# Performance work log

Measured on AMD Instinct MI355X. Metric: run time of the kernel, lower is better.

## Reference

```python
import jax, jax.numpy as jnp
import numpy as np

EPS_DISC = 1e-9  # matches mamba_discretization denominator epsilon


def setup_inputs() -> dict:
    key = jax.random.key(0)
    ks = jax.random.split(key, 12)
    L, D, N, W = 2048, 1024, 16, 3
    s = 0.02  # small init scale to keep softplus/exp well-behaved
    u_seq = jax.random.normal(ks[0], (L, D), jnp.float32)
    # A_log = log(-A) with A = randn*0.1 - 1.0  -> log of a value near 1
    A_log = jnp.log(jnp.clip(1.0 - 0.1 * jax.random.normal(ks[1], (N,), jnp.float32), 0.5, 1.5))
    dt_w = jax.random.normal(ks[2], (D, D), jnp.float32) * s
    dt_b = jax.random.normal(ks[3], (D,), jnp.float32) * s
    B_w = jax.random.normal(ks[4], (N, D), jnp.float32) * s
    B_b = jax.random.normal(ks[5], (N,), jnp.float32) * s
    C_w = jax.random.normal(ks[6], (N, D), jnp.float32) * s
    C_b = jax.random.normal(ks[7], (N,), jnp.float32) * s
    D_w = jnp.ones((D,), jnp.float32)
    scale = jnp.ones((), jnp.float32)
    init_w = jax.random.normal(ks[8], (D * N, D * W), jnp.float32) * s
    init_b = jax.random.normal(ks[9], (D * N,), jnp.float32) * s
    return {"u_seq": u_seq, "A_log": A_log, "dt_w": dt_w, "dt_b": dt_b,
            "B_w": B_w, "B_b": B_b, "C_w": C_w, "C_b": C_b,
            "D_w": D_w, "scale": scale, "init_w": init_w, "init_b": init_b}


def reference(u_seq, A_log, dt_w, dt_b, B_w, B_b, C_w, C_b, D_w, scale, init_w, init_b):
    L, D = u_seq.shape
    N = A_log.shape[0]
    init_window = init_w.shape[1] // D
    # Initial state h0 = init_estimator(u[:W].flatten()).view(D, N)
    u_prefix = u_seq[:init_window].reshape(-1)
    h0 = (u_prefix @ init_w.T + init_b).reshape(D, N)
    # Input-dependent SSM parameters (all L timesteps at once)
    dt = jax.nn.softplus(u_seq @ dt_w.T + dt_b)           # [L, D]
    B = u_seq @ B_w.T + B_b                               # [L, N]
    C = u_seq @ C_w.T + C_b                               # [L, N]
    A = -jnp.exp(A_log)                                   # [N]
    dtA = dt[:, :, None] * A                              # [L, D, N]
    dA = jnp.exp(dtA)                                     # [L, D, N]
    dB = jnp.expm1(dtA) / (dtA + EPS_DISC) * B[:, None, :]  # ZOH discretization
    Bu = dB * u_seq[:, :, None]                           # [L, D, N]

    # Sequential selective-scan recurrence: h_t = dA_t * h_{t-1} + Bu_t
    def step(h, inp):
        dA_t, Bu_t = inp
        h = dA_t * h + Bu_t
        return h, h

    _, h_hist = jax.lax.scan(step, h0, (dA, Bu))          # [L, D, N]
    y_raw = jnp.einsum('ln,ldn->ld', C, h_hist) + D_w * u_seq
    return jax.nn.softplus(y_raw) * jnp.maximum(scale, 0.5)
```

## Files before the change

### kernel.cpp

```cpp
#include <hip/hip_runtime.h>
#include <hip/hip_bf16.h>

typedef __attribute__((ext_vector_type(8))) short short8v;
typedef __attribute__((ext_vector_type(4))) float f32x4;

#define L_SEQ 2048
#define D_DIM 1024
#define N_DIM 16
#define T_CHUNK 32
#define NCHUNK (L_SEQ / T_CHUNK)
#define EPS_DISC 1e-9f

__device__ __forceinline__ float softplusf(float x) {
    return (x > 15.f) ? x : __logf(1.f + __expf(x));
}

__device__ __forceinline__ unsigned short f2bf(float f) {
    unsigned int u = __float_as_uint(f);
    u += 0x7FFFu + ((u >> 16) & 1u);
    return (unsigned short)(u >> 16);
}
__device__ __forceinline__ unsigned int pack2(float a, float b) {
    return (unsigned int)f2bf(a) | ((unsigned int)f2bf(b) << 16);
}
__device__ __forceinline__ float dot4(float4 a, float4 b) {
    return a.x * b.x + a.y * b.y + a.z * b.z + a.w * b.w;
}
__device__ __forceinline__ float dot4v(f32x4 a, f32x4 b) {
    return a.x * b.x + a.y * b.y + a.z * b.z + a.w * b.w;
}

__global__ __launch_bounds__(256, 4) void k_params(const float* __restrict__ u,
                                                   const float* __restrict__ dt_w,
                                                   const float* __restrict__ dt_b,
                                                   const float* __restrict__ B_w,
                                                   const float* __restrict__ B_b,
                                                   const float* __restrict__ C_w,
                                                   const float* __restrict__ C_b,
                                                   const float* __restrict__ init_w,
                                                   const float* __restrict__ init_b,
                                                   float* __restrict__ dt,
                                                   float* __restrict__ Bm,
                                                   float* __restrict__ Cm,
                                                   float* __restrict__ h0) {
    __shared__ unsigned int smem[3072];
    const int b = blockIdx.x;
    const int t = threadIdx.x;
    const int r3 = b % 3;

    if (r3 != 2) {
        const int m = 2 * (b / 3) + r3;
        const int wv = t >> 6, lane = t & 63;
        const int r0 = m * 16 + wv * 4;
        const f32x4* u4 = (const f32x4*)u;
        f32x4 uu[12];
#pragma unroll
        for (int i = 0; i < 12; ++i) uu[i] = u4[i * 64 + lane];
        float rs[4];
#pragma unroll
        for (int j = 0; j < 4; ++j) {
            const f32x4* w4 = (const f32x4*)init_w + (size_t)(r0 + j) * 768;
            f32x4 wr[12];
#pragma unroll
            for (int i = 0; i < 12; ++i)
                wr[i] = __builtin_nontemporal_load(&w4[i * 64 + lane]);
            float s0 = 0.f, s1 = 0.f, s2 = 0.f;
#pragma unroll
            for (int i = 0; i < 4; ++i) {
                s0 += dot4v(wr[i], uu[i]);
                s1 += dot4v(wr[i + 4], uu[i + 4]);
                s2 += dot4v(wr[i + 8], uu[i + 8]);
            }
            rs[j] = s0 + s1 + s2;
        }
#pragma unroll
        for (int j = 0; j < 4; ++j)
#pragma unroll
            for (int mm = 32; mm >= 1; mm >>= 1) rs[j] += __shfl_xor(rs[j], mm);
        if (lane == 0) {
#pragma unroll
            for (int j = 0; j < 4; ++j) h0[r0 + j] = rs[j] + init_b[r0 + j];
        }
        return;
    }

    const int s = b / 3;
    if (s < 256) {
        unsigned int* As = smem;
        unsigned int* Bs = smem + 1024;
        const int bm = s & 31;
        const int bn = s >> 5;
        const int lane = t & 63;
        const int wn   = t >> 6;
        const int lrow = lane & 15, lq = lane >> 4;

        const int arow = t >> 2, aq = t & 3;
        const int brow = t >> 1, bhalf = t & 1;

        const float* uptr = u + (bm * 64 + arow) * 1024 + aq * 8;
        const float* wptr = dt_w + (bn * 128 + brow) * 1024 + bhalf * 16;

        f32x4 acc[4][2];
#pragma unroll
        for (int mi = 0; mi < 4; ++mi)
#pragma unroll
            for (int ni = 0; ni < 2; ++ni) acc[mi][ni] = (f32x4){0.f, 0.f, 0.f, 0.f};

        for (int k0 = 0; k0 < 1024; k0 += 32) {
            __syncthreads();
            {
                const float4* p = (const float4*)(uptr + k0);
                float4 a0 = p[0], a1 = p[1];
                uint4 ca = make_uint4(pack2(a0.x, a0.y), pack2(a0.z, a0.w),
                                      pack2(a1.x, a1.y), pack2(a1.z, a1.w));
                const int akb = aq ^ ((arow >> 1) & 3);
                *(uint4*)&As[arow * 16 + akb * 4] = ca;

                const float4* q = (const float4*)(wptr + k0);
                float4 b0 = q[0], b1 = q[1], b2 = q[2], b3 = q[3];
                uint4 d0 = make_uint4(pack2(b0.x, b0.y), pack2(b0.z, b0.w),
                                      pack2(b1.x, b1.y), pack2(b1.z, b1.w));
                uint4 d1 = make_uint4(pack2(b2.x, b2.y), pack2(b2.z, b2.w),
                                      pack2(b3.x, b3.y), pack2(b3.z, b3.w));
                const int bswz = (brow >> 1) & 3;
                const int kb0 = (bhalf * 2) ^ bswz, kb1 = (bhalf * 2 + 1) ^ bswz;
                *(uint4*)&Bs[brow * 16 + kb0 * 4] = d0;
                *(uint4*)&Bs[brow * 16 + kb1 * 4] = d1;
            }
            __syncthreads();
            short8v af[4], bf[2];
#pragma unroll
            for (int mi = 0; mi < 4; ++mi) {
                const int ar = mi * 16 + lrow;
                const int kb = lq ^ ((ar >> 1) & 3);
                af[mi] = *(const short8v*)&As[ar * 16 + kb * 4];
            }
#pragma unroll
            for (int ni = 0; ni < 2; ++ni) {
                const int br = wn * 32 + ni * 16 + lrow;
                const int kb = lq ^ ((br >> 1) & 3);
                bf[ni] = *(const short8v*)&Bs[br * 16 + kb * 4];
            }
#pragma unroll
            for (int mi = 0; mi < 4; ++mi)
#pragma unroll
                for (int ni = 0; ni < 2; ++ni)
                    acc[mi][ni] = __builtin_amdgcn_mfma_f32_16x16x32_bf16(af[mi], bf[ni], acc[mi][ni], 0, 0, 0);
        }

#pragma unroll
        for (int mi = 0; mi < 4; ++mi)
#pragma unroll
            for (int ni = 0; ni < 2; ++ni) {
                const int cg = bn * 128 + wn * 32 + ni * 16 + lrow;
                const float bv = dt_b[cg];
#pragma unroll
                for (int j = 0; j < 4; ++j) {
                    const int rg = bm * 64 + mi * 16 + lq * 4 + j;
                    dt[rg * 1024 + cg] = softplusf(acc[mi][ni][j] + bv);
                }
            }
    } else {
        const int s2 = s - 256;
        const int wv = t >> 6, lane = t & 63;
#pragma unroll
        for (int rep = 0; rep < 2; ++rep) {
            const int l = s2 * 8 + wv * 2 + rep;
            const float4* u4 = (const float4*)(u + l * 1024);
            float4 ur[4];
#pragma unroll
            for (int i = 0; i < 4; ++i) ur[i] = u4[i * 64 + lane];
#pragma unroll 4
            for (int c = 0; c < 32; ++c) {
                const float4* wr = (const float4*)((c < 16) ? (B_w + c * 1024)
                                                            : (C_w + (c - 16) * 1024));
                float sv = 0.f;
#pragma unroll
                for (int i = 0; i < 4; ++i) sv += dot4(ur[i], wr[i * 64 + lane]);
#pragma unroll
                for (int off = 32; off > 0; off >>= 1) sv += __shfl_down(sv, off);
                if (lane == 0) {
                    if (c < 16) Bm[l * 16 + c] = sv + B_b[c];
                    else        Cm[l * 16 + (c - 16)] = sv + C_b[c - 16];
                }
            }
        }
    }
}

__global__ __launch_bounds__(256) void k_p1(const float* __restrict__ dt,
                                            const float* __restrict__ Bm,
                                            const float* __restrict__ u,
                                            const float* __restrict__ A_log,
                                            float* __restrict__ ap,
                                            float* __restrict__ hl) {
    const int t    = threadIdx.x;
    const int c    = blockIdx.x >> 3;
    const int dblk = blockIdx.x & 7;
    const int dd   = t >> 1;
    const int nh   = t & 1;
    const int d    = dblk * 128 + dd;
    float An[8];
#pragma unroll
    for (int n = 0; n < 8; ++n) An[n] = -__expf(A_log[nh * 8 + n]);
    float h[8], p[8];
#pragma unroll
    for (int n = 0; n < 8; ++n) { h[n] = 0.f; p[n] = 1.f; }

    const int l0 = c * T_CHUNK;
    for (int i = 0; i < T_CHUNK; ++i) {
        const int l = l0 + i;
        const float dtld = dt[l * D_DIM + d];
        const float uld  = u[l * D_DIM + d];
        const float4 b0 = *(const float4*)&Bm[l * 16 + nh * 8];
        const float4 b1 = *(const float4*)&Bm[l * 16 + nh * 8 + 4];
        auto body = [&](int n, float bn) {
            const float x = dtld * An[n];
            const float e = __expf(x);
            const float coef = (e - 1.f) * __builtin_amdgcn_rcpf(x + EPS_DISC);
            const float bu = coef * bn * uld;
            p[n] *= e;
            h[n] = fmaf(e, h[n], bu);
        };
        body(0, b0.x); body(1, b0.y); body(2, b0.z); body(3, b0.w);
        body(4, b1.x); body(5, b1.y); body(6, b1.z); body(7, b1.w);
    }
    const int base = c * (D_DIM * N_DIM) + d * 16 + nh * 8;
    *(float4*)&ap[base + 0] = make_float4(p[0], p[1], p[2], p[3]);
    *(float4*)&ap[base + 4] = make_float4(p[4], p[5], p[6], p[7]);
    *(float4*)&hl[base + 0] = make_float4(h[0], h[1], h[2], h[3]);
    *(float4*)&hl[base + 4] = make_float4(h[4], h[5], h[6], h[7]);
}

__global__ __launch_bounds__(64) void k_p2(const float* __restrict__ h0,
                                           float* __restrict__ ap,
                                           const float* __restrict__ hl) {
    const int ch = blockIdx.x * 64 + threadIdx.x;
    float h = h0[ch];
#pragma unroll 8
    for (int c = 0; c < NCHUNK; ++c) {
        const int idx = c * (D_DIM * N_DIM) + ch;
        const float a = ap[idx];
        const float b = hl[idx];
        ap[idx] = h;
        h = fmaf(a, h, b);
    }
}

__global__ __launch_bounds__(256) void k_p3(const float* __restrict__ dt,
                                            const float* __restrict__ Bm,
                                            const float* __restrict__ Cm,
                                            const float* __restrict__ u,
                                            const float* __restrict__ A_log,
                                            const float* __restrict__ hstart,
                                            const float* __restrict__ D_w,
                                            const float* __restrict__ scale,
                                            float* __restrict__ out) {
    const int t    = threadIdx.x;
    const int c    = blockIdx.x >> 3;
    const int dblk = blockIdx.x & 7;
    const int dd   = t >> 1;
    const int nh   = t & 1;
    const int d    = dblk * 128 + dd;
    float An[8];
#pragma unroll
    for (int n = 0; n < 8; ++n) An[n] = -__expf(A_log[nh * 8 + n]);
    float h[8];
    const int base = c * (D_DIM * N_DIM) + d * 16 + nh * 8;
    {
        float4 h0v = *(const float4*)&hstart[base + 0];
        float4 h1v = *(const float4*)&hstart[base + 4];
        h[0] = h0v.x; h[1] = h0v.y; h[2] = h0v.z; h[3] = h0v.w;
        h[4] = h1v.x; h[5] = h1v.y; h[6] = h1v.z; h[7] = h1v.w;
    }
    const float scl = fmaxf(scale[0], 0.5f);
    const float dw = D_w[d];
    const int l0 = c * T_CHUNK;
    for (int i = 0; i < T_CHUNK; ++i) {
        const int l = l0 + i;
        const float dtld = dt[l * D_DIM + d];
        const float uld  = u[l * D_DIM + d];
        const float4 b0 = *(const float4*)&Bm[l * 16 + nh * 8];
        const float4 b1 = *(const float4*)&Bm[l * 16 + nh * 8 + 4];
        const float4 c0 = *(const float4*)&Cm[l * 16 + nh * 8];
        const float4 c1 = *(const float4*)&Cm[l * 16 + nh * 8 + 4];
        float y = 0.f;
        auto body = [&](int n, float bn, float cn) {
            const float x = dtld * An[n];
            const float e = __expf(x);
            const float coef = (e - 1.f) * __builtin_amdgcn_rcpf(x + EPS_DISC);
            const float bu = coef * bn * uld;
            h[n] = fmaf(e, h[n], bu);
            y = fmaf(cn, h[n], y);
        };
        body(0, b0.x, c0.x); body(1, b0.y, c0.y); body(2, b0.z, c0.z); body(3, b0.w, c0.w);
        body(4, b1.x, c1.x); body(5, b1.y, c1.y); body(6, b1.z, c1.z); body(7, b1.w, c1.w);
        y += __shfl_xor(y, 1);
        if (nh == 0) {
            const float yv = fmaf(dw, uld, y);
            out[l * D_DIM + d] = softplusf(yv) * scl;
        }
    }
}

extern "C" void kernel_launch(void* const* d_in, const int* in_sizes, int n_in,
                              void* d_out, int out_size, void* d_ws, size_t ws_size,
                              hipStream_t stream) {
    const float* u      = (const float*)d_in[0];
    const float* A_log  = (const float*)d_in[1];
    const float* dt_w   = (const float*)d_in[2];
    const float* dt_b   = (const float*)d_in[3];
    const float* B_w    = (const float*)d_in[4];
    const float* B_b    = (const float*)d_in[5];
    const float* C_w    = (const float*)d_in[6];
    const float* C_b    = (const float*)d_in[7];
    const float* D_w    = (const float*)d_in[8];
    const float* scale  = (const float*)d_in[9];
    const float* init_w = (const float*)d_in[10];
    const float* init_b = (const float*)d_in[11];
    float* out = (float*)d_out;

    float* ws = (float*)d_ws;
    float* dt = ws;
    float* Bm = dt + 2097152;
    float* Cm = Bm + 32768;
    float* h0 = Cm + 32768;
    float* ap = h0 + 16384;
    float* hl = ap + 1048576;

    hipLaunchKernelGGL(k_params, dim3(1536), dim3(256), 0, stream,
                       u, dt_w, dt_b, B_w, B_b, C_w, C_b, init_w, init_b,
                       dt, Bm, Cm, h0);
    hipLaunchKernelGGL(k_p1, dim3(512), dim3(256), 0, stream, dt, Bm, u, A_log, ap, hl);
    hipLaunchKernelGGL(k_p2, dim3(256), dim3(64), 0, stream, h0, ap, hl);
    hipLaunchKernelGGL(k_p3, dim3(512), dim3(256), 0, stream, dt, Bm, Cm, u, A_log, ap, D_w, scale, out);
}
```

Baseline: 119.2 us.

## Stream init_w through LDS with async double-buffered global_load_lds for h0 GEMV

Replaces the interleaved block mapping (two init-GEMV blocks per dt-GEMM block) with contiguous block ranges, and rewrites the h0 GEMV so each block handles a 16-row slab. Weight rows are copied into a double-buffered LDS staging area with direct global-to-LDS loads, and the next chunk is prefetched while the current one is reduced. This aims to hide latency on the 200MB init_w stream, which dominates memory traffic. In exchange, LDS per block grows to about 45KB and the launch_bounds occupancy hint is dropped, which may lower occupancy for the dt-GEMM blocks.

After: 111.2 us, median of 2. 6.7% less time.

```diff
diff --git a/kernel.cpp b/kernel.cpp
--- a/kernel.cpp
+++ b/kernel.cpp
@@ -30,66 +30,35 @@
     return a.x * b.x + a.y * b.y + a.z * b.z + a.w * b.w;
 }
 
-__global__ __launch_bounds__(256, 4) void k_params(const float* __restrict__ u,
-                                                   const float* __restrict__ dt_w,
-                                                   const float* __restrict__ dt_b,
-                                                   const float* __restrict__ B_w,
-                                                   const float* __restrict__ B_b,
-                                                   const float* __restrict__ C_w,
-                                                   const float* __restrict__ C_b,
-                                                   const float* __restrict__ init_w,
-                                                   const float* __restrict__ init_b,
-                                                   float* __restrict__ dt,
-                                                   float* __restrict__ Bm,
-                                                   float* __restrict__ Cm,
-                                                   float* __restrict__ h0) {
-    __shared__ unsigned int smem[3072];
+__device__ __forceinline__ void gll16(const float* g, float* lds) {
+    __builtin_amdgcn_global_load_lds(
+        (const __attribute__((address_space(1))) unsigned int*)g,
+        (__attribute__((address_space(3))) unsigned int*)lds,
+        16, 0, 0);
+}
+
+__global__ __launch_bounds__(256) void k_params(const float* __restrict__ u,
+                                                const float* __restrict__ dt_w,
+                                                const float* __restrict__ dt_b,
+                                                const float* __restrict__ B_w,
+                                                const float* __restrict__ B_b,
+                                                const float* __restrict__ C_w,
+                                                const float* __restrict__ C_b,
+                                                const float* __restrict__ init_w,
+                                                const float* __restrict__ init_b,
+                                                float* __restrict__ dt,
+                                                float* __restrict__ Bm,
+                                                float* __restrict__ Cm,
+                                                float* __restrict__ h0) {
+    __shared__ __align__(16) float smem_f[11392];
     const int b = blockIdx.x;
     const int t = threadIdx.x;
-    const int r3 = b % 3;
-
-    if (r3 != 2) {
-        const int m = 2 * (b / 3) + r3;
-        const int wv = t >> 6, lane = t & 63;
-        const int r0 = m * 16 + wv * 4;
-        const f32x4* u4 = (const f32x4*)u;
-        f32x4 uu[12];
-#pragma unroll
-        for (int i = 0; i < 12; ++i) uu[i] = u4[i * 64 + lane];
-        float rs[4];
-#pragma unroll
-        for (int j = 0; j < 4; ++j) {
-            const f32x4* w4 = (const f32x4*)init_w + (size_t)(r0 + j) * 768;
-            f32x4 wr[12];
-#pragma unroll
-            for (int i = 0; i < 12; ++i)
-                wr[i] = __builtin_nontemporal_load(&w4[i * 64 + lane]);
-            float s0 = 0.f, s1 = 0.f, s2 = 0.f;
-#pragma unroll
-            for (int i = 0; i < 4; ++i) {
-                s0 += dot4v(wr[i], uu[i]);
-                s1 += dot4v(wr[i + 4], uu[i + 4]);
-                s2 += dot4v(wr[i + 8], uu[i + 8]);
-            }
-            rs[j] = s0 + s1 + s2;
-        }
-#pragma unroll
-        for (int j = 0; j < 4; ++j)
-#pragma unroll
-            for (int mm = 32; mm >= 1; mm >>= 1) rs[j] += __shfl_xor(rs[j], mm);
-        if (lane == 0) {
-#pragma unroll
-            for (int j = 0; j < 4; ++j) h0[r0 + j] = rs[j] + init_b[r0 + j];
-        }
-        return;
-    }
-
-    const int s = b / 3;
-    if (s < 256) {
-        unsigned int* As = smem;
-        unsigned int* Bs = smem + 1024;
-        const int bm = s & 31;
-        const int bn = s >> 5;
+
+    if (b < 256) {
+        unsigned int* As = (unsigned int*)smem_f;
+        unsigned int* Bs = (unsigned int*)smem_f + 1024;
+        const int bm = b & 31;
+        const int bn = b >> 5;
         const int lane = t & 63;
         const int wn   = t >> 6;
         const int lrow = lane & 15, lq = lane >> 4;
@@ -160,8 +129,8 @@
                     dt[rg * 1024 + cg] = softplusf(acc[mi][ni][j] + bv);
                 }
             }
-    } else {
-        const int s2 = s - 256;
+    } else if (b < 512) {
+        const int s2 = b - 256;
         const int wv = t >> 6, lane = t & 63;
 #pragma unroll
         for (int rep = 0; rep < 2; ++rep) {
@@ -184,6 +153,64 @@
                     else        Cm[l * 16 + (c - 16)] = sv + C_b[c - 16];
                 }
             }
+        }
+    } else {
+        const int slab = b - 512;
+        const int wv = t >> 6, lane = t & 63;
+        float* u_lds = smem_f;
+        float* wbuf0 = smem_f + 3072;
+        float* wbuf1 = smem_f + 3072 + 4160;
+
+#pragma unroll
+        for (int i = 0; i < 3; ++i) {
+            const int idx = wv * 3 + i;
+            gll16(u + idx * 256 + lane * 4, u_lds + idx * 256);
+        }
+#pragma unroll
+        for (int j = 0; j < 4; ++j) {
+            const int r = wv * 4 + j;
+            gll16(init_w + (size_t)(slab * 16 + r) * 3072 + lane * 4,
+                  wbuf0 + r * 260);
+        }
+
+        float acc = 0.f;
+        const int r = t >> 4;
+        const int g = t & 15;
+
+#pragma unroll 1
+        for (int c = 0; c < 12; ++c) {
+            if (c < 11) {
+                float* nb = ((c + 1) & 1) ? wbuf1 : wbuf0;
+#pragma unroll
+                for (int j = 0; j < 4; ++j) {
+                    const int rr = wv * 4 + j;
+                    gll16(init_w + (size_t)(slab * 16 + rr) * 3072 + (c + 1) * 256 + lane * 4,
+                          nb + rr * 260);
+                }
+                asm volatile("s_waitcnt vmcnt(4)" ::: "memory");
+            } else {
+                asm volatile("s_waitcnt vmcnt(0)" ::: "memory");
+            }
+            __builtin_amdgcn_s_barrier();
+
+            const float* wb = ((c & 1) ? wbuf1 : wbuf0) + r * 260;
+            const float* ub = u_lds + c * 256;
+#pragma unroll
+            for (int it = 0; it < 4; ++it) {
+                const int ks = g * 4 + it * 64;
+                f32x4 wv4 = *(const f32x4*)&wb[ks];
+                f32x4 uv4 = *(const f32x4*)&ub[ks];
+                acc += dot4v(wv4, uv4);
+            }
+            asm volatile("" ::: "memory");
+            __builtin_amdgcn_s_barrier();
+        }
+
+#pragma unroll
+        for (int m = 8; m >= 1; m >>= 1) acc += __shfl_xor(acc, m, 16);
+        if (g == 0) {
+            const int row = slab * 16 + r;
+            h0[row] = acc + init_b[row];
         }
     }
 }
```

## Split fused params kernel into separate init matvec and GEMM kernels

Applied to the files above, without the earlier changes.

Splits the combined k_params kernel, which interleaved the init_w matvec blocks with the dt GEMM and B/C projection blocks, into two launches. The new k_mv uses 8192 blocks, each computing two h0 rows with block-wide reduction through shared memory. k_gemm_bc then runs the dt GEMM and the B/C projections alone. The intent is better bandwidth utilisation for the 200MB init_w stream and simpler scheduling of each part. The cost is an extra kernel launch and the loss of overlap between the memory-bound matvec and the compute-bound GEMM.

Result: slower. 127.2 us (+6.7%).

```diff
diff --git a/kernel.cpp b/kernel.cpp
--- a/kernel.cpp
+++ b/kernel.cpp
@@ -26,70 +26,65 @@
 __device__ __forceinline__ float dot4(float4 a, float4 b) {
     return a.x * b.x + a.y * b.y + a.z * b.z + a.w * b.w;
 }
-__device__ __forceinline__ float dot4v(f32x4 a, f32x4 b) {
-    return a.x * b.x + a.y * b.y + a.z * b.z + a.w * b.w;
-}
-
-__global__ __launch_bounds__(256, 4) void k_params(const float* __restrict__ u,
-                                                   const float* __restrict__ dt_w,
-                                                   const float* __restrict__ dt_b,
-                                                   const float* __restrict__ B_w,
-                                                   const float* __restrict__ B_b,
-                                                   const float* __restrict__ C_w,
-                                                   const float* __restrict__ C_b,
-                                                   const float* __restrict__ init_w,
-                                                   const float* __restrict__ init_b,
-                                                   float* __restrict__ dt,
-                                                   float* __restrict__ Bm,
-                                                   float* __restrict__ Cm,
-                                                   float* __restrict__ h0) {
+
+__global__ __launch_bounds__(256, 4) void k_mv(const float* __restrict__ u,
+                                               const float* __restrict__ init_w,
+                                               const float* __restrict__ init_b,
+                                               float* __restrict__ h0) {
+    __shared__ float red[8];
+    const int slab = blockIdx.x;
+    const int t = threadIdx.x;
+    const int wv = t >> 6, lane = t & 63;
+
+    const float4* u4 = (const float4*)u;
+    const float4 u0 = u4[t];
+    const float4 u1 = u4[t + 256];
+    const float4 u2 = u4[t + 512];
+
+    const float4* w4 = (const float4*)init_w + (size_t)slab * 1536;
+    const float4 w0 = w4[t];
+    const float4 w1 = w4[t + 256];
+    const float4 w2 = w4[t + 512];
+    const float4 w3 = w4[t + 768];
+    const float4 w4v = w4[t + 1024];
+    const float4 w5 = w4[t + 1280];
+
+    float acc0 = dot4(w0, u0) + dot4(w1, u1) + dot4(w2, u2);
+    float acc1 = dot4(w3, u0) + dot4(w4v, u1) + dot4(w5, u2);
+
+#pragma unroll
+    for (int m = 32; m >= 1; m >>= 1) {
+        acc0 += __shfl_down(acc0, m);
+        acc1 += __shfl_down(acc1, m);
+    }
+    if (lane == 0) { red[wv] = acc0; red[wv + 4] = acc1; }
+    __syncthreads();
+    if (t < 2) {
+        const float s = red[t * 4 + 0] + red[t * 4 + 1] + red[t * 4 + 2] + red[t * 4 + 3];
+        const int row = slab * 2 + t;
+        h0[row] = s + init_b[row];
+    }
+}
+
+__global__ __launch_bounds__(256) void k_gemm_bc(const float* __restrict__ u,
+                                                 const float* __restrict__ dt_w,
+                                                 const float* __restrict__ dt_b,
+                                                 const float* __restrict__ B_w,
+                                                 const float* __restrict__ B_b,
+                                                 const float* __restrict__ C_w,
+                                                 const float* __restrict__ C_b,
+                                                 float* __restrict__ dt,
+                                                 float* __restrict__ Bm,
+                                                 float* __restrict__ Cm) {
     __shared__ unsigned int smem[3072];
     const int b = blockIdx.x;
     const int t = threadIdx.x;
-    const int r3 = b % 3;
-
-    if (r3 != 2) {
-        const int m = 2 * (b / 3) + r3;
-        const int wv = t >> 6, lane = t & 63;
-        const int r0 = m * 16 + wv * 4;
-        const f32x4* u4 = (const f32x4*)u;
-        f32x4 uu[12];
-#pragma unroll
-        for (int i = 0; i < 12; ++i) uu[i] = u4[i * 64 + lane];
-        float rs[4];
-#pragma unroll
-        for (int j = 0; j < 4; ++j) {
-            const f32x4* w4 = (const f32x4*)init_w + (size_t)(r0 + j) * 768;
-            f32x4 wr[12];
-#pragma unroll
-            for (int i = 0; i < 12; ++i)
-                wr[i] = __builtin_nontemporal_load(&w4[i * 64 + lane]);
-            float s0 = 0.f, s1 = 0.f, s2 = 0.f;
-#pragma unroll
-            for (int i = 0; i < 4; ++i) {
-                s0 += dot4v(wr[i], uu[i]);
-                s1 += dot4v(wr[i + 4], uu[i + 4]);
-                s2 += dot4v(wr[i + 8], uu[i + 8]);
-            }
-            rs[j] = s0 + s1 + s2;
-        }
-#pragma unroll
-        for (int j = 0; j < 4; ++j)
-#pragma unroll
-            for (int mm = 32; mm >= 1; mm >>= 1) rs[j] += __shfl_xor(rs[j], mm);
-        if (lane == 0) {
-#pragma unroll
-            for (int j = 0; j < 4; ++j) h0[r0 + j] = rs[j] + init_b[r0 + j];
-        }
-        return;
-    }
-
-    const int s = b / 3;
-    if (s < 256) {
+
+    if (b < 256) {
         unsigned int* As = smem;
         unsigned int* Bs = smem + 1024;
-        const int bm = s & 31;
-        const int bn = s >> 5;
+        const int bm = b & 31;
+        const int bn = b >> 5;
         const int lane = t & 63;
         const int wn   = t >> 6;
         const int lrow = lane & 15, lq = lane >> 4;
@@ -161,7 +156,7 @@
                 }
             }
     } else {
-        const int s2 = s - 256;
+        const int s2 = b - 256;
         const int wv = t >> 6, lane = t & 63;
 #pragma unroll
         for (int rep = 0; rep < 2; ++rep) {
@@ -328,9 +323,9 @@
     float* ap = h0 + 16384;
     float* hl = ap + 1048576;
 
-    hipLaunchKernelGGL(k_params, dim3(1536), dim3(256), 0, stream,
-                       u, dt_w, dt_b, B_w, B_b, C_w, C_b, init_w, init_b,
-                       dt, Bm, Cm, h0);
+    hipLaunchKernelGGL(k_mv,      dim3(8192), dim3(256), 0, stream, u, init_w, init_b, h0);
+    hipLaunchKernelGGL(k_gemm_bc, dim3(512),  dim3(256), 0, stream,
+                       u, dt_w, dt_b, B_w, B_b, C_w, C_b, dt, Bm, Cm);
     hipLaunchKernelGGL(k_p1, dim3(512), dim3(256), 0, stream, dt, Bm, u, A_log, ap, hl);
     hipLaunchKernelGGL(k_p2, dim3(256), dim3(64), 0, stream, h0, ap, hl);
     hipLaunchKernelGGL(k_p3, dim3(512), dim3(256), 0, stream, dt, Bm, Cm, u, A_log, ap, D_w, scale, out);
```
